# Kernel optimization log

Hardware: AMD Instinct MI355X
Metric: run time of the kernel (lower is better)

The kernel has to match this reference:

```python
import jax, jax.numpy as jnp
import numpy as np

NUM_BLOCKS = 8
SPARSITY = 0.01
HARD_FRAC = 1.0
LN_EPS = 1e-5


def layer_norm(x, w, b):
    mu = jnp.mean(x, axis=-1, keepdims=True)
    var = jnp.mean(jnp.square(x - mu), axis=-1, keepdims=True)
    return (x - mu) * jax.lax.rsqrt(var + LN_EPS) * w + b


def softshrink(v, lam):
    return jnp.sign(v) * jnp.maximum(jnp.abs(v) - lam, 0.0)


def afno2d(x, w1, b1, w2, b2):
    # x: [B,H,W,C] float32
    bias = x
    B, H, W, C = x.shape
    nb = NUM_BLOCKS
    bs = C // nb
    xf = jnp.fft.rfft2(x, axes=(1, 2), norm='ortho')  # [B,H,W//2+1,C] complex
    Wf = W // 2 + 1
    xf = xf.reshape(B, H, Wf, nb, bs)
    total_modes = H // 2 + 1
    kept = int(total_modes * HARD_FRAC)
    lo = total_modes - kept
    hi = min(H, total_modes + kept)
    xs = xf[:, lo:hi, :kept]  # [B,hs,kept,nb,bs]
    xr, xi = xs.real, xs.imag
    o1r = jax.nn.relu(jnp.einsum('bhwki,kio->bhwko', xr, w1[0])
                      - jnp.einsum('bhwki,kio->bhwko', xi, w1[1]) + b1[0])
    o1i = jax.nn.relu(jnp.einsum('bhwki,kio->bhwko', xi, w1[0])
                      + jnp.einsum('bhwki,kio->bhwko', xr, w1[1]) + b1[1])
    o2r = (jnp.einsum('bhwko,koi->bhwki', o1r, w2[0])
           - jnp.einsum('bhwko,koi->bhwki', o1i, w2[1]) + b2[0])
    o2i = (jnp.einsum('bhwko,koi->bhwki', o1i, w2[0])
           + jnp.einsum('bhwko,koi->bhwki', o1r, w2[1]) + b2[1])
    o2r = softshrink(o2r, SPARSITY)
    o2i = softshrink(o2i, SPARSITY)
    oc = o2r + 1j * o2i
    full = jnp.zeros((B, H, Wf, nb, bs), dtype=oc.dtype)
    full = full.at[:, lo:hi, :kept].set(oc)
    full = full.reshape(B, H, Wf, C)
    out = jnp.fft.irfft2(full, s=(H, W), axes=(1, 2), norm='ortho')
    return out + bias


def setup_inputs() -> dict:
    key = jax.random.key(0)
    ks = jax.random.split(key, 12)
    B, H, W, C = 2, 90, 180, 768
    nb = NUM_BLOCKS
    bs = C // nb
    hidden = 4 * C
    scale = 0.02
    return {
        'x': jax.random.normal(ks[0], (B, H, W, C), jnp.float32),
        'norm1_w': jnp.ones((C,), jnp.float32),
        'norm1_b': jnp.zeros((C,), jnp.float32),
        'w1': scale * jax.random.normal(ks[1], (2, nb, bs, bs), jnp.float32),
        'b1': scale * jax.random.normal(ks[2], (2, nb, bs), jnp.float32),
        'w2': scale * jax.random.normal(ks[3], (2, nb, bs, bs), jnp.float32),
        'b2': scale * jax.random.normal(ks[4], (2, nb, bs), jnp.float32),
        'norm2_w': jnp.ones((C,), jnp.float32),
        'norm2_b': jnp.zeros((C,), jnp.float32),
        'fc1_w': jax.random.normal(ks[5], (C, hidden), jnp.float32) * (1.0 / np.sqrt(C)),
        'fc1_b': jnp.zeros((hidden,), jnp.float32),
        'fc2_w': jax.random.normal(ks[6], (hidden, C), jnp.float32) * (1.0 / np.sqrt(hidden)),
        'fc2_b': jnp.zeros((C,), jnp.float32),
    }


def reference(x, norm1_w, norm1_b, w1, b1, w2, b2, norm2_w, norm2_b,
              fc1_w, fc1_b, fc2_w, fc2_b):
    residual = x
    h = layer_norm(x, norm1_w, norm1_b)
    h = afno2d(h, w1, b1, w2, b2)
    # double_skip=True
    h = h + residual
    residual = h
    h = layer_norm(h, norm2_w, norm2_b)
    h = jax.nn.gelu(h @ fc1_w + fc1_b, approximate=False)
    h = h @ fc2_w + fc2_b
    return h + residual
```

## Files before the change

### kernel.cpp

```cpp
#include <hip/hip_runtime.h>
#include <hip/hip_bf16.h>

#define B_    2
#define H_    90
#define W_    180
#define C_    768
#define WFK   46
#define NBK   8
#define BSK   96
#define HID   3072
#define NTOK  (B_*H_*W_)
#define MPAD  32512
#define NPOS  (B_*H_*WFK)
#define LAM   0.01f

typedef __attribute__((ext_vector_type(8))) short short8;
typedef __attribute__((ext_vector_type(4))) float f32x4;

__device__ __forceinline__ float bf2f(short u) {
    union { unsigned int i; float f; } z;
    z.i = ((unsigned int)(unsigned short)u) << 16;
    return z.f;
}

__device__ __forceinline__ void gload_lds16(const void* g, void* l) {
    __builtin_amdgcn_global_load_lds((const __attribute__((address_space(1))) void*)g,
                                     (__attribute__((address_space(3))) void*)l, 16, 0, 0);
}

__device__ __forceinline__ float gelu_f(float v) {
    float u = v * (0.7978845608028654f + 0.03567740813636141f * v * v);
    float au = fabsf(u);
    float e = __expf(2.f * au);
    float t = 1.f - 2.f / (e + 1.f);
    t = copysignf(t, u);
    return 0.5f * v * (1.f + t);
}

__global__ __launch_bounds__(256) void init_tables_kernel(__hip_bfloat16* Tw, __hip_bfloat16* Twf,
                                                          __hip_bfloat16* Thf, __hip_bfloat16* Thi) {
    int i = blockIdx.x * 256 + threadIdx.x;
    const float S = 0.00785674201318386f;
    if (i < 192 * 96) {
        int w = i / 96, k = i % 96;
        int j = k >> 1, odd = k & 1;
        float val = 0.f;
        if (w < W_ && j < WFK) {
            float th = (float)((w * j) % W_) * (float)(6.283185307179586476925286766559 / 180.0);
            if (odd) val = (j == 0) ? 0.f : -2.f * S * sinf(th);
            else     val = (j == 0) ? S : 2.f * S * cosf(th);
        }
        Tw[i] = __float2bfloat16(val);
    }
    if (i < 96 * 192) {
        int r = i / 192, w = i % 192;
        int wf = r >> 1, odd = r & 1;
        float val = 0.f;
        if (w < W_ && wf < WFK) {
            float th = (float)((w * wf) % W_) * (float)(6.283185307179586476925286766559 / 180.0);
            val = odd ? -S * sinf(th) : S * cosf(th);
        }
        Twf[i] = __float2bfloat16(val);
    }
    if (i < 192 * 192) {
        int r = i / 192, j = i % 192;
        float vf = 0.f, vi = 0.f;
        if (r < 180 && j < 180) {
            int k = r >> 1, ro = r & 1, h = j >> 1, jo = j & 1;
            float th = (float)((k * h) % H_) * (float)(6.283185307179586476925286766559 / 90.0);
            float c = cosf(th), s = sinf(th);
            vf = ro ? (jo ? c : -s) : (jo ? s : c);
            vi = ro ? (jo ? c : s) : (jo ? -s : c);
        }
        Thf[i] = __float2bfloat16(vf);
        Thi[i] = __float2bfloat16(vi);
    }
}

__global__ __launch_bounds__(256) void wprep_kernel(
        const float* __restrict__ w1, const float* __restrict__ b1,
        const float* __restrict__ w2, const float* __restrict__ b2,
        __hip_bfloat16* __restrict__ wbig, float* __restrict__ bbig)
{
    int idx = blockIdx.x * 256 + threadIdx.x;
    if (idx < 2 * NBK * 192 * 192) {
        int k = idx % 192;
        int o = (idx / 192) % 192;
        int nb = (idx / (192 * 192)) % NBK;
        int L = idx / (192 * 192 * NBK);
        const float* w = L ? w2 : w1;
        const float* wr = w + (size_t)nb * BSK * BSK;
        const float* wi = w + (size_t)(NBK + nb) * BSK * BSK;
        int kk = k % BSK, oo = o % BSK;
        float val;
        if (o < BSK)  val = (k < BSK) ? wr[kk * BSK + oo] : -wi[kk * BSK + oo];
        else          val = (k < BSK) ? wi[kk * BSK + oo] :  wr[kk * BSK + oo];
        wbig[((size_t)(L * NBK + nb) * 192 + o) * 192 + k] = __float2bfloat16(val);
    }
    if (idx < 2 * NBK * 192) {
        int o = idx % 192;
        int nb = (idx / 192) % NBK;
        int L = idx / (192 * NBK);
        const float* b = L ? b2 : b1;
        bbig[idx] = (o < BSK) ? b[nb * BSK + o] : b[(NBK + nb) * BSK + (o - BSK)];
    }
}

__global__ __launch_bounds__(256) void ln_kernel(const float* __restrict__ in,
        const float* __restrict__ w, const float* __restrict__ b,
        __hip_bfloat16* __restrict__ outb, int ntok_valid)
{
    int tok = blockIdx.x;
    int tid = threadIdx.x;
    size_t base = (size_t)tok * C_;
    if (tok >= ntok_valid) {
        __hip_bfloat16 z = __float2bfloat16(0.f);
        outb[base + tid] = z; outb[base + tid + 256] = z; outb[base + tid + 512] = z;
        return;
    }
    float x0 = in[base + tid], x1 = in[base + tid + 256], x2 = in[base + tid + 512];
    float s = x0 + x1 + x2;
    float q = x0*x0 + x1*x1 + x2*x2;
#pragma unroll
    for (int off = 32; off > 0; off >>= 1) { s += __shfl_down(s, off); q += __shfl_down(q, off); }
    __shared__ float rs[4], rq[4];
    int wid = tid >> 6, lane = tid & 63;
    if (lane == 0) { rs[wid] = s; rq[wid] = q; }
    __syncthreads();
    float ts = rs[0] + rs[1] + rs[2] + rs[3];
    float tq = rq[0] + rq[1] + rq[2] + rq[3];
    float mu = ts * (1.f / C_);
    float var = tq * (1.f / C_) - mu * mu;
    float rstd = rsqrtf(var + 1e-5f);
#pragma unroll
    for (int k = 0; k < 3; ++k) {
        int c = tid + k * 256;
        float xv = (k == 0 ? x0 : (k == 1 ? x1 : x2));
        outb[base + c] = __float2bfloat16((xv - mu) * rstd * w[c] + b[c]);
    }
}

__global__ __launch_bounds__(256) void wfft_kernel(const __hip_bfloat16* __restrict__ h1,
        float* __restrict__ f1r, float* __restrict__ f1i,
        const __hip_bfloat16* __restrict__ Twf)
{
    __shared__ __hip_bfloat16 Xt[64 * 200];
    int slab = blockIdx.x;
    int c0 = blockIdx.y * 64;
    int tid = threadIdx.x, wid = tid >> 6, lane = tid & 63;
    int lrow = lane & 15, lk8 = lane >> 4;
    const short* src = (const short*)h1 + (size_t)slab * W_ * C_ + c0;
    short* X = (short*)Xt;
    for (int i = tid; i < W_ * 8; i += 256) {
        int w = i >> 3, c8 = (i & 7) * 8;
        short8 v = *(const short8*)&src[(size_t)w * C_ + c8];
#pragma unroll
        for (int j = 0; j < 8; ++j) X[(c8 + j) * 200 + w] = v[j];
    }
    for (int z = tid; z < 64 * 12; z += 256) {
        int c = z / 12, w = 180 + z % 12;
        Xt[c * 200 + w] = __float2bfloat16(0.f);
    }
    __syncthreads();
    const short* Tp = (const short*)Twf;
    f32x4 zero = {0.f, 0.f, 0.f, 0.f};
    f32x4 acc[6];
#pragma unroll
    for (int m = 0; m < 6; ++m) acc[m] = zero;
#pragma unroll
    for (int ks = 0; ks < 6; ++ks) {
        short8 bf = *(const short8*)&X[(wid * 16 + lrow) * 200 + ks * 32 + lk8 * 8];
#pragma unroll
        for (int m = 0; m < 6; ++m) {
            short8 af = *(const short8*)&Tp[(m * 16 + lrow) * 192 + ks * 32 + lk8 * 8];
            acc[m] = __builtin_amdgcn_mfma_f32_16x16x32_bf16(af, bf, acc[m], 0, 0, 0);
        }
    }
    int crow = (lane >> 4) * 4, ccol = lane & 15;
#pragma unroll
    for (int m = 0; m < 6; ++m)
#pragma unroll
        for (int j = 0; j < 4; ++j) {
            int r = m * 16 + crow + j;
            int wf = r >> 1;
            if (wf >= WFK) continue;
            size_t o = ((size_t)slab * WFK + wf) * C_ + c0 + wid * 16 + ccol;
            if (r & 1) f1i[o] = acc[m][j];
            else       f1r[o] = acc[m][j];
        }
}

__global__ __launch_bounds__(256) void hdft_kernel(float* __restrict__ dr, float* __restrict__ di,
        const __hip_bfloat16* __restrict__ Th)
{
    __shared__ __hip_bfloat16 Xt[64 * 200];
    int bwf = blockIdx.x;
    int b = bwf / WFK, wf = bwf % WFK;
    int c0 = blockIdx.y * 64;
    int tid = threadIdx.x, wid = tid >> 6, lane = tid & 63;
    int lrow = lane & 15, lk8 = lane >> 4;
    size_t base = ((size_t)(b * H_) * WFK + wf) * C_ + c0;
    short* X = (short*)Xt;
    for (int i = tid; i < H_ * 16; i += 256) {
        int h = i >> 4, cq = (i & 15) * 4;
        size_t a = base + (size_t)h * WFK * C_ + cq;
        float4 re = *(const float4*)&dr[a];
        float4 im = *(const float4*)&di[a];
        X[(cq + 0) * 200 + 2 * h]     = (short)__bfloat16_as_ushort(__float2bfloat16(re.x));
        X[(cq + 0) * 200 + 2 * h + 1] = (short)__bfloat16_as_ushort(__float2bfloat16(im.x));
        X[(cq + 1) * 200 + 2 * h]     = (short)__bfloat16_as_ushort(__float2bfloat16(re.y));
        X[(cq + 1) * 200 + 2 * h + 1] = (short)__bfloat16_as_ushort(__float2bfloat16(im.y));
        X[(cq + 2) * 200 + 2 * h]     = (short)__bfloat16_as_ushort(__float2bfloat16(re.z));
        X[(cq + 2) * 200 + 2 * h + 1] = (short)__bfloat16_as_ushort(__float2bfloat16(im.z));
        X[(cq + 3) * 200 + 2 * h]     = (short)__bfloat16_as_ushort(__float2bfloat16(re.w));
        X[(cq + 3) * 200 + 2 * h + 1] = (short)__bfloat16_as_ushort(__float2bfloat16(im.w));
    }
    for (int z = tid; z < 64 * 12; z += 256) {
        int c = z / 12, j = 180 + z % 12;
        Xt[c * 200 + j] = __float2bfloat16(0.f);
    }
    __syncthreads();
    const short* Tp = (const short*)Th;
    f32x4 zero = {0.f, 0.f, 0.f, 0.f};
    f32x4 acc[3][4];
#pragma unroll
    for (int m = 0; m < 3; ++m)
#pragma unroll
        for (int n = 0; n < 4; ++n) acc[m][n] = zero;
#pragma unroll
    for (int ks = 0; ks < 6; ++ks) {
        short8 af[3], bf[4];
#pragma unroll
        for (int m = 0; m < 3; ++m)
            af[m] = *(const short8*)&Tp[(wid * 48 + m * 16 + lrow) * 192 + ks * 32 + lk8 * 8];
#pragma unroll
        for (int n = 0; n < 4; ++n)
            bf[n] = *(const short8*)&X[(n * 16 + lrow) * 200 + ks * 32 + lk8 * 8];
#pragma unroll
        for (int m = 0; m < 3; ++m)
#pragma unroll
            for (int n = 0; n < 4; ++n)
                acc[m][n] = __builtin_amdgcn_mfma_f32_16x16x32_bf16(af[m], bf[n], acc[m][n], 0, 0, 0);
    }
    int crow = (lane >> 4) * 4, ccol = lane & 15;
#pragma unroll
    for (int m = 0; m < 3; ++m)
#pragma unroll
        for (int j = 0; j < 4; ++j) {
            int r = wid * 48 + m * 16 + crow + j;
            int kh = r >> 1;
            if (kh >= H_) continue;
#pragma unroll
            for (int n = 0; n < 4; ++n) {
                size_t o = base + (size_t)kh * WFK * C_ + n * 16 + ccol;
                if (r & 1) di[o] = acc[m][n][j];
                else       dr[o] = acc[m][n][j];
            }
        }
}

__global__ __launch_bounds__(256) void blockmlp_mfma_kernel(
        float* __restrict__ vr, float* __restrict__ vi,
        const __hip_bfloat16* __restrict__ wbig, const float* __restrict__ bbig)
{
    __shared__ __hip_bfloat16 X1[64 * 200];
    __shared__ __hip_bfloat16 X2[64 * 200];
    int chunk = blockIdx.x;
    int nb = blockIdx.y;
    int tid = threadIdx.x, wid = tid >> 6, lane = tid & 63;
    int p0 = chunk * 64;
    for (int i = tid; i < 64 * 48; i += 256) {
        int p = i / 48, q = i % 48;
        int pg = p0 + p;
        int c4 = (q % 24) * 4;
        bool isr = q < 24;
        float4 v = make_float4(0, 0, 0, 0);
        if (pg < NPOS) {
            const float* src = isr ? vr : vi;
            v = *(const float4*)&src[(size_t)pg * C_ + nb * BSK + c4];
        }
        __hip_bfloat16* d = &X1[p * 200 + (isr ? 0 : 96) + c4];
        d[0] = __float2bfloat16(v.x); d[1] = __float2bfloat16(v.y);
        d[2] = __float2bfloat16(v.z); d[3] = __float2bfloat16(v.w);
    }
    __syncthreads();
    int n0 = wid * 48;
    int lrow = lane & 15, lk8 = lane >> 4;
    int crow = (lane >> 4) * 4, ccol = lane & 15;
    const short* W1 = (const short*)(wbig + (size_t)nb * 192 * 192);
    const short* W2 = (const short*)(wbig + (size_t)(NBK + nb) * 192 * 192);
    const float* bb1 = bbig + nb * 192;
    const float* bb2 = bbig + (NBK + nb) * 192;
    f32x4 zero = {0.f, 0.f, 0.f, 0.f};
    {
        f32x4 acc[4][3];
#pragma unroll
        for (int m = 0; m < 4; ++m)
#pragma unroll
            for (int n = 0; n < 3; ++n) acc[m][n] = zero;
#pragma unroll
        for (int k0 = 0; k0 < 192; k0 += 32) {
            short8 af[4], bf[3];
#pragma unroll
            for (int m = 0; m < 4; ++m)
                af[m] = *(const short8*)&X1[(m * 16 + lrow) * 200 + k0 + lk8 * 8];
#pragma unroll
            for (int n = 0; n < 3; ++n)
                bf[n] = *(const short8*)&W1[(size_t)(n0 + n * 16 + lrow) * 192 + k0 + lk8 * 8];
#pragma unroll
            for (int m = 0; m < 4; ++m)
#pragma unroll
                for (int n = 0; n < 3; ++n)
                    acc[m][n] = __builtin_amdgcn_mfma_f32_16x16x32_bf16(af[m], bf[n], acc[m][n], 0, 0, 0);
        }
        __syncthreads();
#pragma unroll
        for (int m = 0; m < 4; ++m)
#pragma unroll
            for (int j = 0; j < 4; ++j) {
                int row = m * 16 + crow + j;
#pragma unroll
                for (int n = 0; n < 3; ++n) {
                    int col = n0 + n * 16 + ccol;
                    float v = acc[m][n][j] + bb1[col];
                    X2[row * 200 + col] = __float2bfloat16(fmaxf(v, 0.f));
                }
            }
    }
    __syncthreads();
    {
        f32x4 acc[4][3];
#pragma unroll
        for (int m = 0; m < 4; ++m)
#pragma unroll
            for (int n = 0; n < 3; ++n) acc[m][n] = zero;
#pragma unroll
        for (int k0 = 0; k0 < 192; k0 += 32) {
            short8 af[4], bf[3];
#pragma unroll
            for (int m = 0; m < 4; ++m)
                af[m] = *(const short8*)&X2[(m * 16 + lrow) * 200 + k0 + lk8 * 8];
#pragma unroll
            for (int n = 0; n < 3; ++n)
                bf[n] = *(const short8*)&W2[(size_t)(n0 + n * 16 + lrow) * 192 + k0 + lk8 * 8];
#pragma unroll
            for (int m = 0; m < 4; ++m)
#pragma unroll
                for (int n = 0; n < 3; ++n)
                    acc[m][n] = __builtin_amdgcn_mfma_f32_16x16x32_bf16(af[m], bf[n], acc[m][n], 0, 0, 0);
        }
#pragma unroll
        for (int m = 0; m < 4; ++m)
#pragma unroll
            for (int j = 0; j < 4; ++j) {
                int row = m * 16 + crow + j;
                int pg = p0 + row;
                if (pg >= NPOS) continue;
#pragma unroll
                for (int n = 0; n < 3; ++n) {
                    int col = n0 + n * 16 + ccol;
                    float v = acc[m][n][j] + bb2[col];
                    v = v > LAM ? v - LAM : (v < -LAM ? v + LAM : 0.f);
                    if (col < BSK) vr[(size_t)pg * C_ + nb * BSK + col] = v;
                    else           vi[(size_t)pg * C_ + nb * BSK + col - BSK] = v;
                }
            }
    }
}

__global__ __launch_bounds__(256) void iwfft_kernel(
        const float* __restrict__ inr, const float* __restrict__ ini,
        const __hip_bfloat16* __restrict__ h1, const float* __restrict__ x,
        float* __restrict__ out, const __hip_bfloat16* __restrict__ Tw)
{
    __shared__ __hip_bfloat16 Yt[64 * 104];
    int slab = blockIdx.x;
    int c0 = blockIdx.y * 64;
    int tid = threadIdx.x, wid = tid >> 6, lane = tid & 63;
    int lrow = lane & 15, lk8 = lane >> 4;
    size_t sb = (size_t)slab * WFK * C_ + c0;
    for (int i = tid; i < WFK * 16; i += 256) {
        int wf = i >> 4, cq = (i & 15) * 4;
        size_t a = sb + (size_t)wf * C_ + cq;
        float4 vrv = *(const float4*)&inr[a];
        float4 viv = *(const float4*)&ini[a];
        Yt[(cq + 0) * 104 + 2 * wf]     = __float2bfloat16(vrv.x);
        Yt[(cq + 0) * 104 + 2 * wf + 1] = __float2bfloat16(viv.x);
        Yt[(cq + 1) * 104 + 2 * wf]     = __float2bfloat16(vrv.y);
        Yt[(cq + 1) * 104 + 2 * wf + 1] = __float2bfloat16(viv.y);
        Yt[(cq + 2) * 104 + 2 * wf]     = __float2bfloat16(vrv.z);
        Yt[(cq + 2) * 104 + 2 * wf + 1] = __float2bfloat16(viv.z);
        Yt[(cq + 3) * 104 + 2 * wf]     = __float2bfloat16(vrv.w);
        Yt[(cq + 3) * 104 + 2 * wf + 1] = __float2bfloat16(viv.w);
    }
    {
        int c = tid >> 2, kk = 92 + (tid & 3);
        Yt[c * 104 + kk] = __float2bfloat16(0.f);
    }
    __syncthreads();
    const short* Tp = (const short*)Tw;
    f32x4 zero = {0.f, 0.f, 0.f, 0.f};
    f32x4 acc[3][4];
#pragma unroll
    for (int m = 0; m < 3; ++m)
#pragma unroll
        for (int n = 0; n < 4; ++n) acc[m][n] = zero;
#pragma unroll
    for (int ks = 0; ks < 3; ++ks) {
        short8 af[3], bf[4];
#pragma unroll
        for (int m = 0; m < 3; ++m)
            af[m] = *(const short8*)&Tp[(wid * 48 + m * 16 + lrow) * 96 + ks * 32 + lk8 * 8];
#pragma unroll
        for (int n = 0; n < 4; ++n)
            bf[n] = *(const short8*)&Yt[(n * 16 + lrow) * 104 + ks * 32 + lk8 * 8];
#pragma unroll
        for (int m = 0; m < 3; ++m)
#pragma unroll
            for (int n = 0; n < 4; ++n)
                acc[m][n] = __builtin_amdgcn_mfma_f32_16x16x32_bf16(af[m], bf[n], acc[m][n], 0, 0, 0);
    }
    int crow = (lane >> 4) * 4, ccol = lane & 15;
    const short* hp = (const short*)h1;
#pragma unroll
    for (int m = 0; m < 3; ++m)
#pragma unroll
        for (int j = 0; j < 4; ++j) {
            int w = wid * 48 + m * 16 + crow + j;
            if (w >= W_) continue;
            size_t o = ((size_t)slab * W_ + w) * C_ + c0;
#pragma unroll
            for (int n = 0; n < 4; ++n) {
                int col = n * 16 + ccol;
                out[o + col] = acc[m][n][j] + bf2f(hp[o + col]) + x[o + col];
            }
        }
}

__global__ __launch_bounds__(256) void transpose_cvt_kernel(const float* __restrict__ Wm,
        __hip_bfloat16* __restrict__ Wt, int R, int Ccol)
{
    __shared__ float tile[32][33];
    int c0 = blockIdx.x * 32, r0 = blockIdx.y * 32;
    int tid = threadIdx.x;
    int tc = tid & 31, tr = tid >> 5;
#pragma unroll
    for (int k = 0; k < 4; ++k)
        tile[tr + k * 8][tc] = Wm[(size_t)(r0 + tr + k * 8) * Ccol + c0 + tc];
    __syncthreads();
    int rr = tid & 31, cc = tid >> 5;
#pragma unroll
    for (int k = 0; k < 4; ++k)
        Wt[(size_t)(c0 + cc + k * 8) * R + r0 + rr] = __float2bfloat16(tile[rr][cc + k * 8]);
}

template<int EPI>
__global__ __launch_bounds__(256) void gemm_kernel(
        const short* __restrict__ A, const short* __restrict__ Bt,
        const float* __restrict__ bias,
        __hip_bfloat16* __restrict__ obf, float* __restrict__ of32,
        const float* __restrict__ res, int N, int K, int mvalid, int MT, int NT)
{
    __shared__ short As[3][128 * 32];
    __shared__ short Bs[3][128 * 32];
    int id = blockIdx.x;
    const int SUPER = 16;
    int per = SUPER * NT;
    int sidx = id / per;
    int offs = id % per;
    int rows = MT - sidx * SUPER; if (rows > SUPER) rows = SUPER;
    int mt = sidx * SUPER + offs % rows;
    int nt = offs / rows;
    size_t m0 = (size_t)mt * 128, n0 = (size_t)nt * 128;

    int tid = threadIdx.x;
    int wid = tid >> 6, lane = tid & 63;
    int wm = (wid >> 1) * 64, wn = (wid & 1) * 64;
    int lrow = lane & 15, lk8 = lane >> 4;
    f32x4 zero = {0.f, 0.f, 0.f, 0.f};
    f32x4 acc[4][4];
#pragma unroll
    for (int i = 0; i < 4; ++i)
#pragma unroll
        for (int j = 0; j < 4; ++j) acc[i][j] = zero;
    int srow = tid >> 2;
    int scol = ((tid & 3) ^ ((srow >> 1) & 3)) * 8;
    const short* Ag = A + (m0 + srow) * K + scol;
    const short* Bg = Bt + (n0 + srow) * K + scol;
    int ldsoff = tid * 16;
    int rswz = (lk8 ^ ((lrow >> 1) & 3)) * 8;

    auto stage = [&](int buf, int t) {
        const short* Ak = Ag + (size_t)t * 32;
        const short* Bk = Bg + (size_t)t * 32;
        char* ab = (char*)&As[buf][0] + ldsoff;
        char* bb = (char*)&Bs[buf][0] + ldsoff;
        gload_lds16(Ak, ab);
        gload_lds16(Ak + (size_t)64 * K, ab + 4096);
        gload_lds16(Bk, bb);
        gload_lds16(Bk + (size_t)64 * K, bb + 4096);
    };
    auto compute = [&](int buf) {
        short8 af[4], bfr[4];
#pragma unroll
        for (int mf = 0; mf < 4; ++mf) af[mf] = *(const short8*)&As[buf][(wm + mf * 16 + lrow) * 32 + rswz];
#pragma unroll
        for (int nf = 0; nf < 4; ++nf) bfr[nf] = *(const short8*)&Bs[buf][(wn + nf * 16 + lrow) * 32 + rswz];
#pragma unroll
        for (int mf = 0; mf < 4; ++mf)
#pragma unroll
            for (int nf = 0; nf < 4; ++nf)
                acc[mf][nf] = __builtin_amdgcn_mfma_f32_16x16x32_bf16(af[mf], bfr[nf], acc[mf][nf], 0, 0, 0);
    };

    int nk = K / 32;
    stage(0, 0); stage(1, 1); stage(2, 2);
    int cur = 0;
    for (int t = 0; t < nk; ++t) {
        if (t < nk - 2)       asm volatile("s_waitcnt vmcnt(8)" ::: "memory");
        else if (t == nk - 2) asm volatile("s_waitcnt vmcnt(4)" ::: "memory");
        else                  asm volatile("s_waitcnt vmcnt(0)" ::: "memory");
        __builtin_amdgcn_sched_barrier(0);
        __builtin_amdgcn_s_barrier();
        __builtin_amdgcn_sched_barrier(0);
        compute(cur);
        asm volatile("s_waitcnt lgkmcnt(0)" ::: "memory");
        __builtin_amdgcn_sched_barrier(0);
        __builtin_amdgcn_s_barrier();
        __builtin_amdgcn_sched_barrier(0);
        if (t + 3 < nk) stage(cur, t + 3);
        cur = cur + 1; if (cur == 3) cur = 0;
    }

    int crow = (lane >> 4) * 4;
    int ccol = lane & 15;
#pragma unroll
    for (int mf = 0; mf < 4; ++mf) {
#pragma unroll
        for (int j = 0; j < 4; ++j) {
            size_t r = m0 + wm + mf * 16 + crow + j;
            if (EPI == 1 && r >= (size_t)mvalid) continue;
#pragma unroll
            for (int nf = 0; nf < 4; ++nf) {
                size_t cidx = n0 + wn + nf * 16 + ccol;
                float v = acc[mf][nf][j] + bias[cidx];
                if (EPI == 0) {
                    obf[r * N + cidx] = __float2bfloat16(gelu_f(v));
                } else {
                    of32[r * N + cidx] = v + res[r * N + cidx];
                }
            }
        }
    }
}

extern "C" void kernel_launch(void* const* d_in, const int* in_sizes, int n_in,
                              void* d_out, int out_size, void* d_ws, size_t ws_size,
                              hipStream_t stream) {
    (void)in_sizes; (void)n_in; (void)out_size;
    const float* x    = (const float*)d_in[0];
    const float* n1w  = (const float*)d_in[1];
    const float* n1b  = (const float*)d_in[2];
    const float* w1   = (const float*)d_in[3];
    const float* b1   = (const float*)d_in[4];
    const float* w2   = (const float*)d_in[5];
    const float* b2   = (const float*)d_in[6];
    const float* n2w  = (const float*)d_in[7];
    const float* n2b  = (const float*)d_in[8];
    const float* fc1w = (const float*)d_in[9];
    const float* fc1b = (const float*)d_in[10];
    const float* fc2w = (const float*)d_in[11];
    const float* fc2b = (const float*)d_in[12];
    float* out = (float*)d_out;

    const size_t fl_region1 = (size_t)MPAD * C_ / 2;
    const size_t fl_f1      = (size_t)2 * NPOS * C_;
    const size_t fl_tb1     = (size_t)MPAD * HID / 2;
    const size_t fl_tb2     = (size_t)127 * 128 * HID / 2;
    const size_t fl_wx      = 2712576 + 4096;
    const size_t need1 = (fl_region1 + fl_tb1 + fl_wx) * 4;
    const size_t need2 = (fl_region1 + ((fl_f1 > fl_tb2) ? fl_f1 : fl_tb2) + fl_wx) * 4;
    int nch = (ws_size >= need1) ? 1 : (ws_size >= need2) ? 2 : 4;
    size_t fl_tb = (nch == 1) ? fl_tb1 : (nch == 2) ? fl_tb2 : 0;
    size_t fl_big = (fl_f1 > fl_tb) ? fl_f1 : fl_tb;

    float* wsf = (float*)d_ws;
    size_t off = 0;
    auto alloc = [&](size_t nfloats) { float* p = wsf + off; off += (nfloats + 63) & ~(size_t)63; return p; };
    float* region1   = alloc(fl_region1);
    float* regionBig = alloc(fl_big);
    __hip_bfloat16* w1t = (__hip_bfloat16*)alloc((size_t)HID * C_ / 2);
    __hip_bfloat16* w2t = (__hip_bfloat16*)alloc((size_t)HID * C_ / 2);
    __hip_bfloat16* wbig = (__hip_bfloat16*)alloc((size_t)2 * NBK * 192 * 192 / 2);
    float* bbig = alloc(2 * NBK * 192);
    __hip_bfloat16* Tw  = (__hip_bfloat16*)alloc(192 * 96 / 2);
    __hip_bfloat16* Twf = (__hip_bfloat16*)alloc(96 * 192 / 2);
    __hip_bfloat16* Thf = (__hip_bfloat16*)alloc(192 * 192 / 2);
    __hip_bfloat16* Thi = (__hip_bfloat16*)alloc(192 * 192 / 2);

    __hip_bfloat16* h1b = (__hip_bfloat16*)region1;
    __hip_bfloat16* h3  = (__hip_bfloat16*)region1;
    float* f1r = regionBig;
    float* f1i = regionBig + (size_t)NPOS * C_;
    __hip_bfloat16* tb  = (__hip_bfloat16*)regionBig;

    init_tables_kernel<<<144, 256, 0, stream>>>(Tw, Twf, Thf, Thi);
    wprep_kernel<<<(2 * NBK * 192 * 192 + 255) / 256, 256, 0, stream>>>(w1, b1, w2, b2, wbig, bbig);
    transpose_cvt_kernel<<<dim3(HID / 32, C_ / 32), 256, 0, stream>>>(fc1w, w1t, C_, HID);
    transpose_cvt_kernel<<<dim3(C_ / 32, HID / 32), 256, 0, stream>>>(fc2w, w2t, HID, C_);

    ln_kernel<<<NTOK, 256, 0, stream>>>(x, n1w, n1b, h1b, NTOK);
    wfft_kernel<<<dim3(B_ * H_, 12), 256, 0, stream>>>(h1b, f1r, f1i, Twf);
    hdft_kernel<<<dim3(B_ * WFK, 12), 256, 0, stream>>>(f1r, f1i, Thf);
    blockmlp_mfma_kernel<<<dim3(130, NBK), 256, 0, stream>>>(f1r, f1i, wbig, bbig);
    hdft_kernel<<<dim3(B_ * WFK, 12), 256, 0, stream>>>(f1r, f1i, Thi);
    iwfft_kernel<<<dim3(B_ * H_, 12), 256, 0, stream>>>(f1r, f1i, h1b, x, out, Tw);
    ln_kernel<<<MPAD, 256, 0, stream>>>(out, n2w, n2b, h3, NTOK);

    int tilesArr[4], ntiles = 0;
    if (nch == 1)      { tilesArr[0] = 254; ntiles = 1; }
    else if (nch == 2) { tilesArr[0] = 127; tilesArr[1] = 127; ntiles = 2; }
    else               { tilesArr[0] = 64; tilesArr[1] = 64; tilesArr[2] = 64; tilesArr[3] = 62; ntiles = 4; }
    int baseT = 0;
    for (int c = 0; c < ntiles; ++c) {
        int tiles = tilesArr[c];
        size_t baseRow = (size_t)baseT * 128;
        gemm_kernel<0><<<tiles * (HID / 128), 256, 0, stream>>>(
            (const short*)(h3 + baseRow * C_), (const short*)w1t, fc1b,
            tb, nullptr, nullptr, HID, C_, 0, tiles, HID / 128);
        gemm_kernel<1><<<tiles * (C_ / 128), 256, 0, stream>>>(
            (const short*)tb, (const short*)w2t, fc2b,
            nullptr, out + baseRow * C_, out + baseRow * C_, C_, HID, NTOK - (int)baseRow, tiles, C_ / 128);
        baseT += tiles;
    }
}
```

Baseline: 777.9 us.

## Replace 128x128 MLP GEMM with 256x256 tile, 512-thread double-buffered kernel

The MLP GEMMs move from 128x128 output tiles with K=32 triple buffering to 256x256 tiles with K=64 double buffering, 8 waves per block, and a new XOR LDS swizzle. MFMA sections are wrapped in s_setprio, and the grouped tile ordering changes from 16 to 4 rows. The aim is more operand reuse per LDS load and less global traffic per FLOP. In exchange it uses 128KB of LDS per block and more accumulator registers, and with 127 M-tiles by 12 or 3 N-tiles the grid is coarser, which can leave CUs idle on the smaller GEMM.

After: 820.0 us. 1.05x slower.

```diff
diff --git a/kernel.cpp b/kernel.cpp
--- a/kernel.cpp
+++ b/kernel.cpp
@@ -455,95 +455,120 @@
 }
 
 template<int EPI>
-__global__ __launch_bounds__(256) void gemm_kernel(
+__global__ __launch_bounds__(512, 2) void gemm256_kernel(
         const short* __restrict__ A, const short* __restrict__ Bt,
         const float* __restrict__ bias,
         __hip_bfloat16* __restrict__ obf, float* __restrict__ of32,
         const float* __restrict__ res, int N, int K, int mvalid, int MT, int NT)
 {
-    __shared__ short As[3][128 * 32];
-    __shared__ short Bs[3][128 * 32];
+    __shared__ short As[2][256 * 64];
+    __shared__ short Bs[2][256 * 64];
     int id = blockIdx.x;
-    const int SUPER = 16;
+    const int SUPER = 4;
     int per = SUPER * NT;
     int sidx = id / per;
     int offs = id % per;
     int rows = MT - sidx * SUPER; if (rows > SUPER) rows = SUPER;
     int mt = sidx * SUPER + offs % rows;
     int nt = offs / rows;
-    size_t m0 = (size_t)mt * 128, n0 = (size_t)nt * 128;
+    size_t m0 = (size_t)mt * 256, n0 = (size_t)nt * 256;
 
     int tid = threadIdx.x;
     int wid = tid >> 6, lane = tid & 63;
-    int wm = (wid >> 1) * 64, wn = (wid & 1) * 64;
-    int lrow = lane & 15, lk8 = lane >> 4;
+    int wmidx = wid >> 2, wnidx = wid & 3;
+    int lrow = lane & 15, lk8 = lane >> 4, l7 = lrow & 7;
+
+    int srow8 = tid >> 3;
+    int soct  = (tid & 7) ^ (srow8 & 7);
+    const short* Ag = A + (m0 + srow8) * K + soct * 8;
+    const short* Bg = Bt + (n0 + srow8) * K + soct * 8;
+    int ldst = srow8 * 128 + (tid & 7) * 16;
+
+    int aoff0 = (wmidx * 128 + lrow) * 128 + ((lk8) ^ l7) * 16;
+    int aoff1 = (wmidx * 128 + lrow) * 128 + ((4 + lk8) ^ l7) * 16;
+    int boff0 = (wnidx * 64 + lrow) * 128 + ((lk8) ^ l7) * 16;
+    int boff1 = (wnidx * 64 + lrow) * 128 + ((4 + lk8) ^ l7) * 16;
+
     f32x4 zero = {0.f, 0.f, 0.f, 0.f};
-    f32x4 acc[4][4];
-#pragma unroll
-    for (int i = 0; i < 4; ++i)
+    f32x4 acc[8][4];
+#pragma unroll
+    for (int i = 0; i < 8; ++i)
 #pragma unroll
         for (int j = 0; j < 4; ++j) acc[i][j] = zero;
-    int srow = tid >> 2;
-    int scol = ((tid & 3) ^ ((srow >> 1) & 3)) * 8;
-    const short* Ag = A + (m0 + srow) * K + scol;
-    const short* Bg = Bt + (n0 + srow) * K + scol;
-    int ldsoff = tid * 16;
-    int rswz = (lk8 ^ ((lrow >> 1) & 3)) * 8;
-
-    auto stage = [&](int buf, int t) {
-        const short* Ak = Ag + (size_t)t * 32;
-        const short* Bk = Bg + (size_t)t * 32;
-        char* ab = (char*)&As[buf][0] + ldsoff;
-        char* bb = (char*)&Bs[buf][0] + ldsoff;
-        gload_lds16(Ak, ab);
-        gload_lds16(Ak + (size_t)64 * K, ab + 4096);
-        gload_lds16(Bk, bb);
-        gload_lds16(Bk + (size_t)64 * K, bb + 4096);
+
+    auto stage = [&](int buf, int kt) {
+        const short* Ak = Ag + (size_t)kt * 64;
+        const short* Bk = Bg + (size_t)kt * 64;
+        char* ab = (char*)&As[buf][0] + ldst;
+        char* bb = (char*)&Bs[buf][0] + ldst;
+#pragma unroll
+        for (int g = 0; g < 4; ++g) {
+            gload_lds16(Ak + (size_t)g * 64 * K, ab + g * 8192);
+            gload_lds16(Bk + (size_t)g * 64 * K, bb + g * 8192);
+        }
     };
-    auto compute = [&](int buf) {
-        short8 af[4], bfr[4];
-#pragma unroll
-        for (int mf = 0; mf < 4; ++mf) af[mf] = *(const short8*)&As[buf][(wm + mf * 16 + lrow) * 32 + rswz];
-#pragma unroll
-        for (int nf = 0; nf < 4; ++nf) bfr[nf] = *(const short8*)&Bs[buf][(wn + nf * 16 + lrow) * 32 + rswz];
-#pragma unroll
-        for (int mf = 0; mf < 4; ++mf)
-#pragma unroll
-            for (int nf = 0; nf < 4; ++nf)
-                acc[mf][nf] = __builtin_amdgcn_mfma_f32_16x16x32_bf16(af[mf], bfr[nf], acc[mf][nf], 0, 0, 0);
-    };
-
-    int nk = K / 32;
-    stage(0, 0); stage(1, 1); stage(2, 2);
-    int cur = 0;
-    for (int t = 0; t < nk; ++t) {
-        if (t < nk - 2)       asm volatile("s_waitcnt vmcnt(8)" ::: "memory");
-        else if (t == nk - 2) asm volatile("s_waitcnt vmcnt(4)" ::: "memory");
-        else                  asm volatile("s_waitcnt vmcnt(0)" ::: "memory");
+
+    int NK = K >> 6;
+    stage(0, 0);
+    for (int T = 0; T < NK; ++T) {
+        int buf = T & 1;
+        if (T + 1 < NK) {
+            stage(buf ^ 1, T + 1);
+            asm volatile("s_waitcnt vmcnt(8)" ::: "memory");
+        } else {
+            asm volatile("s_waitcnt vmcnt(0)" ::: "memory");
+        }
         __builtin_amdgcn_sched_barrier(0);
         __builtin_amdgcn_s_barrier();
         __builtin_amdgcn_sched_barrier(0);
-        compute(cur);
-        asm volatile("s_waitcnt lgkmcnt(0)" ::: "memory");
-        __builtin_amdgcn_sched_barrier(0);
+        {
+            const char* Ab = (const char*)&As[buf][0];
+            const char* Bb = (const char*)&Bs[buf][0];
+            short8 bfr[4][2];
+#pragma unroll
+            for (int nf = 0; nf < 4; ++nf) {
+                bfr[nf][0] = *(const short8*)(Bb + boff0 + nf * 2048);
+                bfr[nf][1] = *(const short8*)(Bb + boff1 + nf * 2048);
+            }
+#pragma unroll
+            for (int mh = 0; mh < 2; ++mh) {
+                short8 af[4][2];
+#pragma unroll
+                for (int mf = 0; mf < 4; ++mf) {
+                    af[mf][0] = *(const short8*)(Ab + aoff0 + (mh * 4 + mf) * 2048);
+                    af[mf][1] = *(const short8*)(Ab + aoff1 + (mh * 4 + mf) * 2048);
+                }
+                asm volatile("s_waitcnt lgkmcnt(0)" ::: "memory");
+                __builtin_amdgcn_sched_barrier(0);
+                __builtin_amdgcn_s_setprio(1);
+#pragma unroll
+                for (int mf = 0; mf < 4; ++mf)
+#pragma unroll
+                    for (int nf = 0; nf < 4; ++nf) {
+                        acc[mh * 4 + mf][nf] = __builtin_amdgcn_mfma_f32_16x16x32_bf16(
+                            af[mf][0], bfr[nf][0], acc[mh * 4 + mf][nf], 0, 0, 0);
+                        acc[mh * 4 + mf][nf] = __builtin_amdgcn_mfma_f32_16x16x32_bf16(
+                            af[mf][1], bfr[nf][1], acc[mh * 4 + mf][nf], 0, 0, 0);
+                    }
+                __builtin_amdgcn_s_setprio(0);
+            }
+        }
         __builtin_amdgcn_s_barrier();
         __builtin_amdgcn_sched_barrier(0);
-        if (t + 3 < nk) stage(cur, t + 3);
-        cur = cur + 1; if (cur == 3) cur = 0;
     }
 
     int crow = (lane >> 4) * 4;
     int ccol = lane & 15;
 #pragma unroll
-    for (int mf = 0; mf < 4; ++mf) {
+    for (int mf8 = 0; mf8 < 8; ++mf8) {
 #pragma unroll
         for (int j = 0; j < 4; ++j) {
-            size_t r = m0 + wm + mf * 16 + crow + j;
+            size_t r = m0 + wmidx * 128 + mf8 * 16 + crow + j;
             if (EPI == 1 && r >= (size_t)mvalid) continue;
 #pragma unroll
             for (int nf = 0; nf < 4; ++nf) {
-                size_t cidx = n0 + wn + nf * 16 + ccol;
-                float v = acc[mf][nf][j] + bias[cidx];
+                size_t cidx = n0 + wnidx * 64 + nf * 16 + ccol;
+                float v = acc[mf8][nf][j] + bias[cidx];
                 if (EPI == 0) {
                     obf[r * N + cidx] = __float2bfloat16(gelu_f(v));
                 } else {
@@ -576,7 +601,7 @@
     const size_t fl_region1 = (size_t)MPAD * C_ / 2;
     const size_t fl_f1      = (size_t)2 * NPOS * C_;
     const size_t fl_tb1     = (size_t)MPAD * HID / 2;
-    const size_t fl_tb2     = (size_t)127 * 128 * HID / 2;
+    const size_t fl_tb2     = (size_t)64 * 256 * HID / 2;
     const size_t fl_wx      = 2712576 + 4096;
     const size_t need1 = (fl_region1 + fl_tb1 + fl_wx) * 4;
     const size_t need2 = (fl_region1 + ((fl_f1 > fl_tb2) ? fl_f1 : fl_tb2) + fl_wx) * 4;
@@ -618,19 +643,19 @@
     ln_kernel<<<MPAD, 256, 0, stream>>>(out, n2w, n2b, h3, NTOK);
 
     int tilesArr[4], ntiles = 0;
-    if (nch == 1)      { tilesArr[0] = 254; ntiles = 1; }
-    else if (nch == 2) { tilesArr[0] = 127; tilesArr[1] = 127; ntiles = 2; }
-    else               { tilesArr[0] = 64; tilesArr[1] = 64; tilesArr[2] = 64; tilesArr[3] = 62; ntiles = 4; }
+    if (nch == 1)      { tilesArr[0] = 127; ntiles = 1; }
+    else if (nch == 2) { tilesArr[0] = 64; tilesArr[1] = 63; ntiles = 2; }
+    else               { tilesArr[0] = 32; tilesArr[1] = 32; tilesArr[2] = 32; tilesArr[3] = 31; ntiles = 4; }
     int baseT = 0;
     for (int c = 0; c < ntiles; ++c) {
         int tiles = tilesArr[c];
-        size_t baseRow = (size_t)baseT * 128;
-        gemm_kernel<0><<<tiles * (HID / 128), 256, 0, stream>>>(
+        size_t baseRow = (size_t)baseT * 256;
+        gemm256_kernel<0><<<tiles * (HID / 256), 512, 0, stream>>>(
             (const short*)(h3 + baseRow * C_), (const short*)w1t, fc1b,
-            tb, nullptr, nullptr, HID, C_, 0, tiles, HID / 128);
-        gemm_kernel<1><<<tiles * (C_ / 128), 256, 0, stream>>>(
+            tb, nullptr, nullptr, HID, C_, 0, tiles, HID / 256);
+        gemm256_kernel<1><<<tiles * (C_ / 256), 512, 0, stream>>>(
             (const short*)tb, (const short*)w2t, fc2b,
-            nullptr, out + baseRow * C_, out + baseRow * C_, C_, HID, NTOK - (int)baseRow, tiles, C_ / 128);
+            nullptr, out + baseRow * C_, out + baseRow * C_, C_, HID, NTOK - (int)baseRow, tiles, C_ / 256);
         baseT += tiles;
     }
 }
```

## Restructure MLP GEMMs to 256x128 tiles with 8 waves and XCD-aware remap

Applied to the files above, without the earlier changes.

The fc1/fc2 GEMM kernel now uses 512-thread workgroups computing 256x128 output tiles with K-steps of 64. It double-buffers across two k-halves, issuing global-to-LDS loads for the next tile while the current one computes, and raises wave priority around the MFMA block. Workgroup IDs are remapped so each XCD gets a contiguous range of tiles, and the super-row grouping drops from 16 to 4. The intent is better operand reuse, better L2 locality per XCD, and more overlap of loads with compute. In exchange it uses much more LDS per workgroup, which limits occupancy to one block per CU.

New measurement: 761.4 us. 1.02x faster.

```diff
diff --git a/kernel.cpp b/kernel.cpp
--- a/kernel.cpp
+++ b/kernel.cpp
@@ -455,81 +455,95 @@
 }
 
 template<int EPI>
-__global__ __launch_bounds__(256) void gemm_kernel(
+__global__ __launch_bounds__(512, 1) void gemm_kernel(
         const short* __restrict__ A, const short* __restrict__ Bt,
         const float* __restrict__ bias,
         __hip_bfloat16* __restrict__ obf, float* __restrict__ of32,
         const float* __restrict__ res, int N, int K, int mvalid, int MT, int NT)
 {
-    __shared__ short As[3][128 * 32];
-    __shared__ short Bs[3][128 * 32];
-    int id = blockIdx.x;
-    const int SUPER = 16;
+    __shared__ short lds[49152];
+    int nwg = MT * NT;
+    int orig = blockIdx.x;
+    int xcd = orig & 7, loc = orig >> 3;
+    int q = nwg >> 3, rm = nwg & 7;
+    int wg = (xcd < rm ? xcd * (q + 1) : rm * (q + 1) + (xcd - rm) * q) + loc;
+    const int SUPER = 4;
     int per = SUPER * NT;
-    int sidx = id / per;
-    int offs = id % per;
+    int sidx = wg / per, offs = wg % per;
     int rows = MT - sidx * SUPER; if (rows > SUPER) rows = SUPER;
     int mt = sidx * SUPER + offs % rows;
     int nt = offs / rows;
-    size_t m0 = (size_t)mt * 128, n0 = (size_t)nt * 128;
+    size_t m0 = (size_t)mt * 256, n0 = (size_t)nt * 128;
 
     int tid = threadIdx.x;
     int wid = tid >> 6, lane = tid & 63;
-    int wm = (wid >> 1) * 64, wn = (wid & 1) * 64;
+    int wmidx = wid >> 1, wnidx = wid & 1;
     int lrow = lane & 15, lk8 = lane >> 4;
+    int rswz = (lk8 ^ ((lrow >> 1) & 3)) * 16;
+
+    int sr = tid >> 2;
+    int soct = (tid & 3) ^ ((sr >> 1) & 3);
+    const short* Agbase = A + (m0 + sr) * (size_t)K + soct * 8;
+    const short* Bgbase = Bt + (n0 + sr) * (size_t)K + soct * 8;
+    int dA = sr * 64 + (tid & 3) * 16;
     f32x4 zero = {0.f, 0.f, 0.f, 0.f};
     f32x4 acc[4][4];
 #pragma unroll
     for (int i = 0; i < 4; ++i)
 #pragma unroll
         for (int j = 0; j < 4; ++j) acc[i][j] = zero;
-    int srow = tid >> 2;
-    int scol = ((tid & 3) ^ ((srow >> 1) & 3)) * 8;
-    const short* Ag = A + (m0 + srow) * K + scol;
-    const short* Bg = Bt + (n0 + srow) * K + scol;
-    int ldsoff = tid * 16;
-    int rswz = (lk8 ^ ((lrow >> 1) & 3)) * 8;
-
-    auto stage = [&](int buf, int t) {
-        const short* Ak = Ag + (size_t)t * 32;
-        const short* Bk = Bg + (size_t)t * 32;
-        char* ab = (char*)&As[buf][0] + ldsoff;
-        char* bb = (char*)&Bs[buf][0] + ldsoff;
-        gload_lds16(Ak, ab);
-        gload_lds16(Ak + (size_t)64 * K, ab + 4096);
-        gload_lds16(Bk, bb);
-        gload_lds16(Bk + (size_t)64 * K, bb + 4096);
+
+    auto stagepair = [&](int buf, int kt, int ksh) {
+        const short* As = Agbase + kt * 64 + ksh * 32;
+        char* Ad = (char*)lds + buf * 32768 + ksh * 16384 + dA;
+        gload_lds16(As, Ad);
+        gload_lds16(As + (size_t)128 * K, Ad + 8192);
+        const short* Bs = Bgbase + kt * 64 + ksh * 32;
+        char* Bd = (char*)lds + 65536 + buf * 16384 + ksh * 8192 + dA;
+        gload_lds16(Bs, Bd);
     };
-    auto compute = [&](int buf) {
+
+    int abase = (wmidx * 64 + lrow) * 64 + rswz;
+    int bbase = 65536 + (wnidx * 64 + lrow) * 64 + rswz;
+    auto phase = [&](int buf, int ks, int kt_stage, bool do_stage, int waitN) {
+        const char* L = (const char*)lds;
         short8 af[4], bfr[4];
-#pragma unroll
-        for (int mf = 0; mf < 4; ++mf) af[mf] = *(const short8*)&As[buf][(wm + mf * 16 + lrow) * 32 + rswz];
-#pragma unroll
-        for (int nf = 0; nf < 4; ++nf) bfr[nf] = *(const short8*)&Bs[buf][(wn + nf * 16 + lrow) * 32 + rswz];
+        int ao = buf * 32768 + ks * 16384 + abase;
+        int bo = buf * 16384 + ks * 8192 + bbase;
+#pragma unroll
+        for (int mf = 0; mf < 4; ++mf) af[mf] = *(const short8*)(L + ao + mf * 1024);
+#pragma unroll
+        for (int nf = 0; nf < 4; ++nf) bfr[nf] = *(const short8*)(L + bo + nf * 1024);
+        if (do_stage) stagepair(buf ^ 1, kt_stage, ks);
+        __builtin_amdgcn_sched_barrier(0);
+        __builtin_amdgcn_s_barrier();
+        asm volatile("s_waitcnt lgkmcnt(0)" ::: "memory");
+        __builtin_amdgcn_sched_barrier(0);
+        __builtin_amdgcn_s_setprio(1);
 #pragma unroll
         for (int mf = 0; mf < 4; ++mf)
 #pragma unroll
             for (int nf = 0; nf < 4; ++nf)
                 acc[mf][nf] = __builtin_amdgcn_mfma_f32_16x16x32_bf16(af[mf], bfr[nf], acc[mf][nf], 0, 0, 0);
-    };
-
-    int nk = K / 32;
-    stage(0, 0); stage(1, 1); stage(2, 2);
-    int cur = 0;
-    for (int t = 0; t < nk; ++t) {
-        if (t < nk - 2)       asm volatile("s_waitcnt vmcnt(8)" ::: "memory");
-        else if (t == nk - 2) asm volatile("s_waitcnt vmcnt(4)" ::: "memory");
-        else                  asm volatile("s_waitcnt vmcnt(0)" ::: "memory");
+        __builtin_amdgcn_s_setprio(0);
+        if (waitN == 0)      asm volatile("s_waitcnt vmcnt(0)" ::: "memory");
+        else if (waitN > 0)  asm volatile("s_waitcnt vmcnt(3)" ::: "memory");
         __builtin_amdgcn_sched_barrier(0);
         __builtin_amdgcn_s_barrier();
         __builtin_amdgcn_sched_barrier(0);
-        compute(cur);
-        asm volatile("s_waitcnt lgkmcnt(0)" ::: "memory");
-        __builtin_amdgcn_sched_barrier(0);
-        __builtin_amdgcn_s_barrier();
-        __builtin_amdgcn_sched_barrier(0);
-        if (t + 3 < nk) stage(cur, t + 3);
-        cur = cur + 1; if (cur == 3) cur = 0;
+    };
+
+    int NK = K >> 6;
+    stagepair(0, 0, 0);
+    stagepair(0, 0, 1);
+    asm volatile("s_waitcnt vmcnt(3)" ::: "memory");
+    __builtin_amdgcn_sched_barrier(0);
+    __builtin_amdgcn_s_barrier();
+    for (int t = 0; t < NK; ++t) {
+        int buf = t & 1;
+        bool last = (t == NK - 1);
+        phase(buf, 0, t + 1, !last, last ? 0 : 1);
+        phase(buf, 1, t + 1, !last, last ? -1 : 1);
     }
 
     int crow = (lane >> 4) * 4;
@@ -538,11 +552,11 @@
     for (int mf = 0; mf < 4; ++mf) {
 #pragma unroll
         for (int j = 0; j < 4; ++j) {
-            size_t r = m0 + wm + mf * 16 + crow + j;
+            size_t r = m0 + wmidx * 64 + mf * 16 + crow + j;
             if (EPI == 1 && r >= (size_t)mvalid) continue;
 #pragma unroll
             for (int nf = 0; nf < 4; ++nf) {
-                size_t cidx = n0 + wn + nf * 16 + ccol;
+                size_t cidx = n0 + wnidx * 64 + nf * 16 + ccol;
                 float v = acc[mf][nf][j] + bias[cidx];
                 if (EPI == 0) {
                     obf[r * N + cidx] = __float2bfloat16(gelu_f(v));
@@ -576,7 +590,7 @@
     const size_t fl_region1 = (size_t)MPAD * C_ / 2;
     const size_t fl_f1      = (size_t)2 * NPOS * C_;
     const size_t fl_tb1     = (size_t)MPAD * HID / 2;
-    const size_t fl_tb2     = (size_t)127 * 128 * HID / 2;
+    const size_t fl_tb2     = (size_t)64 * 256 * HID / 2;
     const size_t fl_wx      = 2712576 + 4096;
     const size_t need1 = (fl_region1 + fl_tb1 + fl_wx) * 4;
     const size_t need2 = (fl_region1 + ((fl_f1 > fl_tb2) ? fl_f1 : fl_tb2) + fl_wx) * 4;
@@ -618,17 +632,17 @@
     ln_kernel<<<MPAD, 256, 0, stream>>>(out, n2w, n2b, h3, NTOK);
 
     int tilesArr[4], ntiles = 0;
-    if (nch == 1)      { tilesArr[0] = 254; ntiles = 1; }
-    else if (nch == 2) { tilesArr[0] = 127; tilesArr[1] = 127; ntiles = 2; }
-    else               { tilesArr[0] = 64; tilesArr[1] = 64; tilesArr[2] = 64; tilesArr[3] = 62; ntiles = 4; }
+    if (nch == 1)      { tilesArr[0] = 127; ntiles = 1; }
+    else if (nch == 2) { tilesArr[0] = 64; tilesArr[1] = 63; ntiles = 2; }
+    else               { tilesArr[0] = 32; tilesArr[1] = 32; tilesArr[2] = 32; tilesArr[3] = 31; ntiles = 4; }
     int baseT = 0;
     for (int c = 0; c < ntiles; ++c) {
         int tiles = tilesArr[c];
-        size_t baseRow = (size_t)baseT * 128;
-        gemm_kernel<0><<<tiles * (HID / 128), 256, 0, stream>>>(
+        size_t baseRow = (size_t)baseT * 256;
+        gemm_kernel<0><<<tiles * (HID / 128), 512, 0, stream>>>(
             (const short*)(h3 + baseRow * C_), (const short*)w1t, fc1b,
             tb, nullptr, nullptr, HID, C_, 0, tiles, HID / 128);
-        gemm_kernel<1><<<tiles * (C_ / 128), 256, 0, stream>>>(
+        gemm_kernel<1><<<tiles * (C_ / 128), 512, 0, stream>>>(
             (const short*)tb, (const short*)w2t, fc2b,
             nullptr, out + baseRow * C_, out + baseRow * C_, C_, HID, NTOK - (int)baseRow, tiles, C_ / 128);
         baseT += tiles;
```
